# Kernel optimization log

Hardware: AMD Instinct MI355X
Metric: run time of the kernel (lower is better)

Reference implementation:

```python
import jax, jax.numpy as jnp
import numpy as np
import math

IMAGE_SIZE = 512
N_ANGLES = 180
BATCH = 4


def _shepp_logan_filter(size):
    # Matches _get_fourier_filter(size, 'shepp-logan') in the torch module.
    n = np.concatenate([np.arange(1, size // 2 + 1, 2), np.arange(size // 2 - 1, 0, -2)])
    f = np.zeros(size, dtype=np.float64)
    f[0] = 0.25
    f[1::2] = -1.0 / (np.pi * n) ** 2
    ff = 2.0 * np.real(np.fft.fft(f))
    omega = np.pi * np.fft.fftfreq(size)[1:]
    ff[1:] *= np.sin(omega) / omega
    return jnp.asarray(ff, dtype=jnp.float32)


def setup_inputs() -> dict:
    key = jax.random.key(0)
    sinogram = jax.random.normal(key, (BATCH, N_ANGLES, IMAGE_SIZE), dtype=jnp.float32)
    return {"sinogram": sinogram}


def _inverse_radon(sinogram):
    B, A, P = sinogram.shape
    S = P  # image_size == proj_size (required by the torch filter expand)
    # --- FFT ramp filtering (pad_size == P for power-of-two P >= 64, so pad_width = 0) ---
    ff = _shepp_logan_filter(P)  # [P]
    filtered = jnp.real(
        jnp.fft.ifft(jnp.fft.fft(sinogram, axis=-1) * ff, axis=-1)
    ).astype(sinogram.dtype)  # [B, A, P]

    # --- backprojection grid (note: x axis is reversed, as in the torch meshgrid) ---
    x = jnp.arange(S - 1, -1, -1, dtype=jnp.float32) - S // 2  # [W]
    y = jnp.arange(S, dtype=jnp.float32) - S // 2              # [H]
    angles_rad = jnp.linspace(0.0, 180.0, A) * (math.pi / 180.0)  # [A]
    half = P // 2

    def body(acc, inp):
        theta, row = inp  # theta scalar, row: [B, P] filtered projection for this angle
        # unnormalized sample position; equals grid_sample(align_corners=True) coord
        p = x[None, :] * jnp.sin(theta) + y[:, None] * jnp.cos(theta) + half  # [H, W]
        i0f = jnp.floor(p)
        frac = p - i0f  # [H, W]
        i0 = i0f.astype(jnp.int32)
        i1 = i0 + 1

        def tap(idx):
            # bilinear tap with zeros padding (out-of-range taps contribute 0)
            valid = (idx >= 0) & (idx <= P - 1)  # [H, W]
            v = jnp.take(row, jnp.clip(idx, 0, P - 1), axis=1)  # [B, H, W]
            return jnp.where(valid[None], v, jnp.zeros((), dtype=row.dtype))

        contrib = (1.0 - frac)[None] * tap(i0) + frac[None] * tap(i1)  # [B, H, W]
        return acc + contrib, None

    out0 = jnp.zeros((B, S, S), dtype=sinogram.dtype)
    out, _ = jax.lax.scan(body, out0, (angles_rad, jnp.swapaxes(filtered, 0, 1)))
    out = out * (math.pi / (2.0 * A))

    # circle mask
    radius = S // 2
    mask = (x[None, :] ** 2 + y[:, None] ** 2) <= radius ** 2  # [H, W]
    out = out * mask[None].astype(out.dtype)
    return out[:, None]  # [B, 1, S, S]


def reference(sinogram):
    return _inverse_radon(sinogram)
```

## Files before the change

kernel.cpp:

```cpp
#include <hip/hip_runtime.h>
#include <math.h>

#define P      512
#define NA     180
#define NB     4
#define FS2    1056
#define FOFF2  16
#define GUARD  512
#define TS     32
#define WSF    100
#define AHALF  90

#if __has_builtin(__builtin_amdgcn_fractf)
#define FRACT(x) __builtin_amdgcn_fractf(x)
#else
#define FRACT(x) ((x) - floorf(x))
#endif

typedef float f4g __attribute__((ext_vector_type(4), aligned(16)));
typedef float f4l __attribute__((ext_vector_type(4), aligned(8)));

__global__ __launch_bounds__(64) void ir_spectrum(float* __restrict__ ffg) {
    const int o = blockIdx.x;
    const int t = threadIdx.x;
    double s = 0.0;
    #pragma unroll
    for (int i = 0; i < 4; ++i) {
        const int m = t + 64 * i;
        const int idx = 2 * m + 1;
        const int n = (idx < 256) ? idx : (512 - idx);
        const double fv = -1.0 / ((M_PI * n) * (M_PI * n));
        const int ph = (o * idx) & 511;
        s += fv * cos((2.0 * M_PI / 512.0) * (double)ph);
    }
    #pragma unroll
    for (int off = 32; off; off >>= 1) s += __shfl_down(s, off, 64);
    if (t == 0) {
        double ff = 0.5 + 2.0 * s;
        if (o > 0) {
            const double freq = (o <= 256) ? (double)o / 512.0 : ((double)o - 512.0) / 512.0;
            const double w = M_PI * freq;
            ff *= sin(w) / w;
        }
        ffg[o] = (float)ff;
    }
}

__global__ __launch_bounds__(64) void ir_impulse(const float* __restrict__ ffg,
                                                 float* __restrict__ hr) {
    const int o = blockIdx.x;
    const int t = threadIdx.x;
    double s = 0.0;
    #pragma unroll
    for (int i = 0; i < 8; ++i) {
        const int k = t + 64 * i;
        const int ph = (o * k) & 511;
        s += (double)ffg[k] * cos((2.0 * M_PI / 512.0) * (double)ph);
    }
    #pragma unroll
    for (int off = 32; off; off >>= 1) s += __shfl_down(s, off, 64);
    if (t == 0) hr[o] = (float)(s / 512.0);
}

__global__ __launch_bounds__(256) void ir_filter(const float* __restrict__ sino,
                                                 const float* __restrict__ hr,
                                                 float* __restrict__ fil2) {
    __shared__ float row2[2][2 * P];
    const int a = blockIdx.x;
    const int p = blockIdx.y;
    const int t = threadIdx.x;
    const int r = t >> 7;
    const int tt = t & 127;
    const int b = 2 * p + r;

    const float* src = sino + ((size_t)b * NA + a) * P;
    const float4 v = *(const float4*)(src + 4 * tt);
    *(float4*)&row2[r][4 * tt] = v;
    *(float4*)&row2[r][4 * tt + P] = v;
    __syncthreads();

    const int base0 = P + 4 * tt;
    float4 A = *(const float4*)&row2[r][base0];
    float a0 = 0.f, a1 = 0.f, a2 = 0.f, a3 = 0.f;
    #pragma unroll 4
    for (int J = 0; J < P; J += 4) {
        const float4 Bv = *(const float4*)&row2[r][base0 - J - 4];
        const float h0 = hr[J], h1 = hr[J + 1], h2v = hr[J + 2], h3 = hr[J + 3];
        a0 = fmaf(h0, A.x, a0); a0 = fmaf(h1, Bv.w, a0); a0 = fmaf(h2v, Bv.z, a0); a0 = fmaf(h3, Bv.y, a0);
        a1 = fmaf(h0, A.y, a1); a1 = fmaf(h1, A.x, a1); a1 = fmaf(h2v, Bv.w, a1); a1 = fmaf(h3, Bv.z, a1);
        a2 = fmaf(h0, A.z, a2); a2 = fmaf(h1, A.y, a2); a2 = fmaf(h2v, A.x, a2); a2 = fmaf(h3, Bv.w, a2);
        a3 = fmaf(h0, A.w, a3); a3 = fmaf(h1, A.z, a3); a3 = fmaf(h2v, A.y, a3); a3 = fmaf(h3, A.x, a3);
        A = Bv;
    }
    float* frow = fil2 + ((size_t)p * NA + a) * FS2;
    const int o0 = FOFF2 + 8 * tt + r;
    frow[o0]     = a0;
    frow[o0 + 2] = a1;
    frow[o0 + 4] = a2;
    frow[o0 + 6] = a3;
    if (t < FOFF2) {
        frow[t] = 0.f;
        frow[FOFF2 + 2 * P + t] = 0.f;
    }
}

__global__ __launch_bounds__(256) void ir_backproject(const float* __restrict__ fil2,
                                                      float* __restrict__ out) {
    __shared__ float4 angc[NA];
    __shared__ float win[AHALF * WSF];

    const int t = threadIdx.x;
    const int lane = t & 63;
    const int wave = t >> 6;
    const int w0 = blockIdx.x * TS, h0 = blockIdx.y * TS;
    const int p = blockIdx.z;

    const int w = w0 + (lane & 15);
    const int h = h0 + (lane >> 4) + 4 * wave;

    const int ix0 = 255 - w, ix1 = ix0 - 16;
    const int iy0 = h - 256, iy1 = iy0 + 16;
    const int r2 = 256 * 256;
    const int m00 = (ix0 * ix0 + iy0 * iy0) <= r2;
    const int m01 = (ix1 * ix1 + iy0 * iy0) <= r2;
    const int m10 = (ix0 * ix0 + iy1 * iy1) <= r2;
    const int m11 = (ix1 * ix1 + iy1 * iy1) <= r2;

    float* o0 = out + (((size_t)(2 * p) * P) + h) * P + w;
    float* o1 = o0 + (size_t)P * P;

    if (__syncthreads_count(m00 | m01 | m10 | m11) == 0) {
        o0[0] = 0.f; o0[16] = 0.f; o0[16 * P] = 0.f; o0[16 * P + 16] = 0.f;
        o1[0] = 0.f; o1[16] = 0.f; o1[16 * P] = 0.f; o1[16 * P + 16] = 0.f;
        return;
    }

    if (t < NA) {
        const float th = (float)t * (float)(M_PI / (double)(NA - 1));
        const float s = sinf(th), c = cosf(th);
        const float xlo = (float)(224 - w0);
        const float ylo = (float)(h0 - 256), yhi = (float)(h0 - 225);
        const float pmin = s * xlo + fminf(c * ylo, c * yhi) + 256.0f;
        const int base = ((int)floorf(pmin) - 2) & ~1;
        angc[t] = make_float4(s, c, (float)(256 - base), (float)base);
    }
    __syncthreads();

    const float xf = (float)ix0;
    const float yf = (float)iy0;
    const float* fbase = fil2 + (size_t)p * NA * FS2;
    float a00 = 0.f, a01 = 0.f, a10 = 0.f, a11 = 0.f;
    float b00 = 0.f, b01 = 0.f, b10 = 0.f, b11 = 0.f;

    #pragma unroll
    for (int half = 0; half < 2; ++half) {
        const int A0 = half * AHALF;

        for (int idx = t; idx < AHALF * (WSF / 4); idx += 256) {
            const int al = idx / (WSF / 4);
            const int i = idx - al * (WSF / 4);
            const int a = A0 + al;
            const int base = (int)angc[a].w;
            const f4g vv = *(const f4g*)(fbase + a * FS2 + FOFF2 + 2 * base + 4 * i);
            *(f4g*)(win + al * WSF + 4 * i) = vv;
        }
        __syncthreads();

        #pragma unroll 2
        for (int al = 0; al < AHALF; ++al) {
            const float4 ac = angc[A0 + al];
            const float q00 = fmaf(xf, ac.x, fmaf(yf, ac.y, ac.z));
            const float q01 = fmaf(-16.f, ac.x, q00);
            const float q10 = fmaf( 16.f, ac.y, q00);
            const float q11 = fmaf( 16.f, ac.y, q01);
            const float* wb = win + al * WSF;
            {
                const int j = (int)q00; const float fr = FRACT(q00);
                const f4l W = *(const f4l*)(wb + 2 * j);
                a00 = fmaf(1.f - fr, W.x, fmaf(fr, W.z, a00));
                b00 = fmaf(1.f - fr, W.y, fmaf(fr, W.w, b00));
            }
            {
                const int j = (int)q01; const float fr = FRACT(q01);
                const f4l W = *(const f4l*)(wb + 2 * j);
                a01 = fmaf(1.f - fr, W.x, fmaf(fr, W.z, a01));
                b01 = fmaf(1.f - fr, W.y, fmaf(fr, W.w, b01));
            }
            {
                const int j = (int)q10; const float fr = FRACT(q10);
                const f4l W = *(const f4l*)(wb + 2 * j);
                a10 = fmaf(1.f - fr, W.x, fmaf(fr, W.z, a10));
                b10 = fmaf(1.f - fr, W.y, fmaf(fr, W.w, b10));
            }
            {
                const int j = (int)q11; const float fr = FRACT(q11);
                const f4l W = *(const f4l*)(wb + 2 * j);
                a11 = fmaf(1.f - fr, W.x, fmaf(fr, W.z, a11));
                b11 = fmaf(1.f - fr, W.y, fmaf(fr, W.w, b11));
            }
        }
        if (half == 0) __syncthreads();
    }

    const float scale = (float)(M_PI / (2.0 * NA));
    o0[0]           = m00 ? a00 * scale : 0.f;
    o0[16]          = m01 ? a01 * scale : 0.f;
    o0[16 * P]      = m10 ? a10 * scale : 0.f;
    o0[16 * P + 16] = m11 ? a11 * scale : 0.f;
    o1[0]           = m00 ? b00 * scale : 0.f;
    o1[16]          = m01 ? b01 * scale : 0.f;
    o1[16 * P]      = m10 ? b10 * scale : 0.f;
    o1[16 * P + 16] = m11 ? b11 * scale : 0.f;
}

extern "C" void kernel_launch(void* const* d_in, const int* in_sizes, int n_in,
                              void* d_out, int out_size, void* d_ws, size_t ws_size,
                              hipStream_t stream) {
    const float* sino = (const float*)d_in[0];
    float* out = (float*)d_out;
    float* ws = (float*)d_ws;

    float* ffg  = ws;
    float* hr   = ws + 512;
    float* fil2 = ws + 1024 + GUARD;

    ir_spectrum<<<P, 64, 0, stream>>>(ffg);
    ir_impulse<<<P, 64, 0, stream>>>(ffg, hr);

    dim3 gridF(NA, NB / 2);
    ir_filter<<<gridF, 256, 0, stream>>>(sino, hr, fil2);

    dim3 gridB(P / TS, P / TS, NB / 2);
    ir_backproject<<<gridB, 256, 0, stream>>>(fil2, out);
}
```

Measured before the change: 115.1 us.

## Shrink backprojection tile to 16x16 with one pixel per thread

The backprojection block now covers a 16x16 tile with one pixel per thread instead of a 32x32 tile with four pixels per thread. The per-angle filtered-sample window shrinks to match and is staged in three segments of 60 angles rather than two of 90. This gives four times as many blocks, which is meant to improve occupancy and load balance and to skip more tiles entirely outside the circle mask. In exchange it loses the per-thread reuse of angle coefficients across four pixels and pays window loads and barriers over more blocks.

```diff
diff --git a/kernel.cpp b/kernel.cpp
--- a/kernel.cpp
+++ b/kernel.cpp
@@ -7,9 +7,9 @@
 #define FS2    1056
 #define FOFF2  16
 #define GUARD  512
-#define TS     32
-#define WSF    100
-#define AHALF  90
+#define TS     16
+#define WSF    56
+#define ASEG   60
 
 #if __has_builtin(__builtin_amdgcn_fractf)
 #define FRACT(x) __builtin_amdgcn_fractf(x)
@@ -107,56 +107,49 @@
 __global__ __launch_bounds__(256) void ir_backproject(const float* __restrict__ fil2,
                                                       float* __restrict__ out) {
     __shared__ float4 angc[NA];
-    __shared__ float win[AHALF * WSF];
+    __shared__ float win[ASEG * WSF];
 
     const int t = threadIdx.x;
-    const int lane = t & 63;
-    const int wave = t >> 6;
     const int w0 = blockIdx.x * TS, h0 = blockIdx.y * TS;
     const int p = blockIdx.z;
 
-    const int w = w0 + (lane & 15);
-    const int h = h0 + (lane >> 4) + 4 * wave;
+    const int w = w0 + (t & 15);
+    const int h = h0 + (t >> 4);
 
-    const int ix0 = 255 - w, ix1 = ix0 - 16;
-    const int iy0 = h - 256, iy1 = iy0 + 16;
-    const int r2 = 256 * 256;
-    const int m00 = (ix0 * ix0 + iy0 * iy0) <= r2;
-    const int m01 = (ix1 * ix1 + iy0 * iy0) <= r2;
-    const int m10 = (ix0 * ix0 + iy1 * iy1) <= r2;
-    const int m11 = (ix1 * ix1 + iy1 * iy1) <= r2;
+    const int ix = 255 - w;
+    const int iy = h - 256;
+    const int m = (ix * ix + iy * iy) <= 256 * 256;
 
     float* o0 = out + (((size_t)(2 * p) * P) + h) * P + w;
     float* o1 = o0 + (size_t)P * P;
 
-    if (__syncthreads_count(m00 | m01 | m10 | m11) == 0) {
-        o0[0] = 0.f; o0[16] = 0.f; o0[16 * P] = 0.f; o0[16 * P + 16] = 0.f;
-        o1[0] = 0.f; o1[16] = 0.f; o1[16 * P] = 0.f; o1[16 * P + 16] = 0.f;
+    if (__syncthreads_count(m) == 0) {
+        o0[0] = 0.f;
+        o1[0] = 0.f;
         return;
     }
 
     if (t < NA) {
         const float th = (float)t * (float)(M_PI / (double)(NA - 1));
         const float s = sinf(th), c = cosf(th);
-        const float xlo = (float)(224 - w0);
-        const float ylo = (float)(h0 - 256), yhi = (float)(h0 - 225);
+        const float xlo = (float)(240 - w0);
+        const float ylo = (float)(h0 - 256), yhi = (float)(h0 - 241);
         const float pmin = s * xlo + fminf(c * ylo, c * yhi) + 256.0f;
         const int base = ((int)floorf(pmin) - 2) & ~1;
         angc[t] = make_float4(s, c, (float)(256 - base), (float)base);
     }
     __syncthreads();
 
-    const float xf = (float)ix0;
-    const float yf = (float)iy0;
+    const float xf = (float)ix;
+    const float yf = (float)iy;
     const float* fbase = fil2 + (size_t)p * NA * FS2;
-    float a00 = 0.f, a01 = 0.f, a10 = 0.f, a11 = 0.f;
-    float b00 = 0.f, b01 = 0.f, b10 = 0.f, b11 = 0.f;
+    float acc0 = 0.f, acc1 = 0.f;
 
     #pragma unroll
-    for (int half = 0; half < 2; ++half) {
-        const int A0 = half * AHALF;
+    for (int seg = 0; seg < 3; ++seg) {
+        const int A0 = seg * ASEG;
 
-        for (int idx = t; idx < AHALF * (WSF / 4); idx += 256) {
+        for (int idx = t; idx < ASEG * (WSF / 4); idx += 256) {
             const int al = idx / (WSF / 4);
             const int i = idx - al * (WSF / 4);
             const int a = A0 + al;
@@ -166,51 +159,22 @@
         }
         __syncthreads();
 
-        #pragma unroll 2
-        for (int al = 0; al < AHALF; ++al) {
+        #pragma unroll 4
+        for (int al = 0; al < ASEG; ++al) {
             const float4 ac = angc[A0 + al];
-            const float q00 = fmaf(xf, ac.x, fmaf(yf, ac.y, ac.z));
-            const float q01 = fmaf(-16.f, ac.x, q00);
-            const float q10 = fmaf( 16.f, ac.y, q00);
-            const float q11 = fmaf( 16.f, ac.y, q01);
-            const float* wb = win + al * WSF;
-            {
-                const int j = (int)q00; const float fr = FRACT(q00);
-                const f4l W = *(const f4l*)(wb + 2 * j);
-                a00 = fmaf(1.f - fr, W.x, fmaf(fr, W.z, a00));
-                b00 = fmaf(1.f - fr, W.y, fmaf(fr, W.w, b00));
-            }
-            {
-                const int j = (int)q01; const float fr = FRACT(q01);
-                const f4l W = *(const f4l*)(wb + 2 * j);
-                a01 = fmaf(1.f - fr, W.x, fmaf(fr, W.z, a01));
-                b01 = fmaf(1.f - fr, W.y, fmaf(fr, W.w, b01));
-            }
-            {
-                const int j = (int)q10; const float fr = FRACT(q10);
-                const f4l W = *(const f4l*)(wb + 2 * j);
-                a10 = fmaf(1.f - fr, W.x, fmaf(fr, W.z, a10));
-                b10 = fmaf(1.f - fr, W.y, fmaf(fr, W.w, b10));
-            }
-            {
-                const int j = (int)q11; const float fr = FRACT(q11);
-                const f4l W = *(const f4l*)(wb + 2 * j);
-                a11 = fmaf(1.f - fr, W.x, fmaf(fr, W.z, a11));
-                b11 = fmaf(1.f - fr, W.y, fmaf(fr, W.w, b11));
-            }
+            const float q = fmaf(xf, ac.x, fmaf(yf, ac.y, ac.z));
+            const int j = (int)q;
+            const float fr = FRACT(q);
+            const f4l W = *(const f4l*)(win + al * WSF + 2 * j);
+            acc0 = fmaf(1.f - fr, W.x, fmaf(fr, W.z, acc0));
+            acc1 = fmaf(1.f - fr, W.y, fmaf(fr, W.w, acc1));
         }
-        if (half == 0) __syncthreads();
+        if (seg < 2) __syncthreads();
     }
 
     const float scale = (float)(M_PI / (2.0 * NA));
-    o0[0]           = m00 ? a00 * scale : 0.f;
-    o0[16]          = m01 ? a01 * scale : 0.f;
-    o0[16 * P]      = m10 ? a10 * scale : 0.f;
-    o0[16 * P + 16] = m11 ? a11 * scale : 0.f;
-    o1[0]           = m00 ? b00 * scale : 0.f;
-    o1[16]          = m01 ? b01 * scale : 0.f;
-    o1[16 * P]      = m10 ? b10 * scale : 0.f;
-    o1[16 * P + 16] = m11 ? b11 * scale : 0.f;
+    o0[0] = m ? acc0 * scale : 0.f;
+    o1[0] = m ? acc1 * scale : 0.f;
 }
 
 extern "C" void kernel_launch(void* const* d_in, const int* in_sizes, int n_in,
```

Measured after the change: 122.7 us. 1.07x slower.
